# Optimization experiments

Hardware: AMD Instinct MI355X
Metric: run time of the kernel (lower is better)

## Reference

```python
import jax, jax.numpy as jnp
import numpy as np

N_NODES = 50000
N_EDGES = 800000
IN_CH = 128
HID = 64
PROJ = 32


def _gcn_norm(edge_index, n):
    # add self loops, symmetric normalization D^-1/2 (A+I) D^-1/2
    loop = jnp.arange(n, dtype=edge_index.dtype)
    src = jnp.concatenate([edge_index[0], loop])
    dst = jnp.concatenate([edge_index[1], loop])
    deg = jax.ops.segment_sum(jnp.ones_like(dst, jnp.float32), dst, num_segments=n)
    dinv = deg ** -0.5  # deg >= 1 due to self loops
    norm = dinv[src] * dinv[dst]
    return src, dst, norm


def _propagate(h, src, dst, norm, n):
    # gather -> scale -> scatter-add (message passing along A_hat)
    return jax.ops.segment_sum(h[src] * norm[:, None], dst, num_segments=n)


def _ho_gcn_layer(x, src, dst, norm, Ws, b, n):
    # out = sum_{k=1..max_order} (A_hat^k x) W_k + b
    out = jnp.zeros((n, Ws[0].shape[1]), x.dtype)
    h = x
    for W in Ws:
        h = _propagate(h, src, dst, norm, n)
        out = out + h @ W
    return out + b


def setup_inputs() -> dict:
    key = jax.random.key(0)
    ks = jax.random.split(key, 16)

    def w(k, fan_in, fan_out):
        return (jax.random.normal(k, (fan_in, fan_out), jnp.float32) / np.sqrt(fan_in)).astype(jnp.float32)

    x = jax.random.normal(ks[0], (N_NODES, IN_CH), jnp.float32)
    edge_index = jax.random.randint(ks[1], (2, N_EDGES), 0, N_NODES, dtype=jnp.int64)
    return {
        "x": x,
        "edge_index": edge_index,
        # conv1: max_order=2 -> two weights
        "W1_1": w(ks[2], IN_CH, HID), "W1_2": w(ks[3], IN_CH, HID),
        "b1": jnp.zeros((HID,), jnp.float32),
        # conv2
        "W2_1": w(ks[4], HID, HID // 2), "W2_2": w(ks[5], HID, HID // 2),
        "b2": jnp.zeros((HID // 2,), jnp.float32),
        # projection head
        "Wp1": w(ks[6], HID // 2, PROJ), "bp1": jnp.zeros((PROJ,), jnp.float32),
        "Wp2": w(ks[7], PROJ, PROJ), "bp2": jnp.zeros((PROJ,), jnp.float32),
        # coordinate head
        "Wc1": w(ks[8], HID // 2, HID // 4), "bc1": jnp.zeros((HID // 4,), jnp.float32),
        "Wc2": w(ks[9], HID // 4, 2), "bc2": jnp.zeros((2,), jnp.float32),
    }


def reference(x, edge_index, W1_1, W1_2, b1, W2_1, W2_2, b2,
              Wp1, bp1, Wp2, bp2, Wc1, bc1, Wc2, bc2):
    n = x.shape[0]
    src, dst, norm = _gcn_norm(edge_index, n)
    h1 = jax.nn.relu(_ho_gcn_layer(x, src, dst, norm, (W1_1, W1_2), b1, n))
    # dropout is identity in eval/reference mode
    h2 = jax.nn.relu(_ho_gcn_layer(h1, src, dst, norm, (W2_1, W2_2), b2, n))
    z = jax.nn.relu(h2 @ Wp1 + bp1) @ Wp2 + bp2
    coordinates = jax.nn.relu(h2 @ Wc1 + bc1) @ Wc2 + bc2
    return (coordinates, z)
```

## Files before the change

kernel.cpp:

```cpp
#include <hip/hip_runtime.h>

#define NN 50000
#define NE 800000
#define S 4
#define BINW 12500
#define NN4 (NN * S)
#define NBLK2 ((NN4 + 255) / 256)
#define NBG ((NN + 63) / 64)
#define NBH4 ((NE / 4 + 255) / 256)
#define COLCAP (NE + 3 * NN4 + 8)

__global__ __launch_bounds__(256) void zero_cnt_k(int* __restrict__ cnt,
                                                  float* __restrict__ dinv,
                                                  float* __restrict__ y1s,
                                                  float* __restrict__ y2s,
                                                  float* __restrict__ z1s,
                                                  float* __restrict__ z2s) {
    int i = blockIdx.x * blockDim.x + threadIdx.x;
    if (i < NN4) cnt[i] = 0;
    if (blockIdx.x == 0) {
        int t = threadIdx.x;
        if (t < 64) { y1s[t] = 0.f; y2s[t] = 0.f; }
        else if (t < 96) { z1s[t - 64] = 0.f; z2s[t - 64] = 0.f; }
        else if (t == 96) dinv[NN] = 0.f;
    }
}

__global__ __launch_bounds__(256) void hist_k(const int* __restrict__ src,
                                              const int* __restrict__ dst,
                                              int* __restrict__ cnt,
                                              int* __restrict__ rank) {
    int e = (blockIdx.x * 256 + threadIdx.x) * 4;
    if (e >= NE) return;
    int4 s4 = *(const int4*)(src + e);
    int4 d4 = *(const int4*)(dst + e);
    int4 r;
    r.x = atomicAdd(&cnt[d4.x * S + s4.x / BINW], 1);
    r.y = atomicAdd(&cnt[d4.y * S + s4.y / BINW], 1);
    r.z = atomicAdd(&cnt[d4.z * S + s4.z / BINW], 1);
    r.w = atomicAdd(&cnt[d4.w * S + s4.w / BINW], 1);
    *(int4*)(rank + e) = r;
}

__global__ __launch_bounds__(256) void sum_blocks_k(const int* __restrict__ cnt,
                                                    int* __restrict__ bsum,
                                                    float* __restrict__ dinv) {
    __shared__ int s[256];
    int t = threadIdx.x;
    int i = blockIdx.x * 256 + t;
    int v = 0;
    if (i < NN4) {
        int c = cnt[i];
        v = (c + 3) & ~3;
        if ((i & 3) == 0) {
            int deg = c + cnt[i + 1] + cnt[i + 2] + cnt[i + 3];
            dinv[i >> 2] = rsqrtf((float)(deg + 1));
        }
    }
    s[t] = v;
    __syncthreads();
    for (int off = 128; off > 0; off >>= 1) {
        if (t < off) s[t] += s[t + off];
        __syncthreads();
    }
    if (t == 0) bsum[blockIdx.x] = s[0];
}

__global__ __launch_bounds__(256) void scan_final_k(const int* __restrict__ cnt,
                                                    const int* __restrict__ bsum,
                                                    int* __restrict__ rowsS) {
    __shared__ int sOff[256];
    __shared__ int s[256];
    int t = threadIdx.x;
    int accum = 0;
    for (int idx = t; idx < NBLK2; idx += 256)
        if (idx < blockIdx.x) accum += bsum[idx];
    sOff[t] = accum;
    __syncthreads();
    for (int off = 128; off > 0; off >>= 1) {
        if (t < off) sOff[t] += sOff[t + off];
        __syncthreads();
    }
    int boff = sOff[0];

    int i = blockIdx.x * 256 + t;
    int v = (i < NN4) ? ((cnt[i] + 3) & ~3) : 0;
    s[t] = v;
    __syncthreads();
    for (int off = 1; off < 256; off <<= 1) {
        int x = (t >= off) ? s[t - off] : 0;
        __syncthreads();
        s[t] += x;
        __syncthreads();
    }
    if (i < NN4) rowsS[i] = boff + s[t] - v;
    if (blockIdx.x == NBLK2 - 1 && t == 255) rowsS[NN4] = boff + s[t];
}

__global__ __launch_bounds__(256) void gemm1_scatter_k(const float* __restrict__ A,
                                                       const float* __restrict__ WA,
                                                       const float* __restrict__ WB,
                                                       float* __restrict__ outA,
                                                       float* __restrict__ outB,
                                                       const int* __restrict__ src,
                                                       const int* __restrict__ dst,
                                                       const int* __restrict__ rank,
                                                       const int* __restrict__ rowsS,
                                                       const int* __restrict__ cnt,
                                                       int* __restrict__ col) {
    if (blockIdx.x >= NBG) {
        int idx = (blockIdx.x - NBG) * 256 + threadIdx.x;
        int e = idx * 4;
        if (e < NE) {
            int4 s4 = *(const int4*)(src + e);
            int4 d4 = *(const int4*)(dst + e);
            int4 r4 = *(const int4*)(rank + e);
            col[rowsS[d4.x * S + s4.x / BINW] + r4.x] = s4.x;
            col[rowsS[d4.y * S + s4.y / BINW] + r4.y] = s4.y;
            col[rowsS[d4.z * S + s4.z / BINW] + r4.z] = s4.z;
            col[rowsS[d4.w * S + s4.w / BINW] + r4.w] = s4.w;
        }
        if (idx < NN4) {
            int end = rowsS[idx] + cnt[idx];
            int nxt = rowsS[idx + 1];
            for (int i = end; i < nxt; i++) col[i] = NN;
        }
        return;
    }

    __shared__ float As[64 * 36];
    __shared__ float W1s[32 * 68];
    __shared__ float W2s[32 * 68];
    const int t = threadIdx.x;
    const int tj = t & 15;
    const int tn = t >> 4;
    const int n0 = blockIdx.x * 64;
    float acc[4][8] = {};

    for (int kc = 0; kc < 128; kc += 32) {
        if (kc) __syncthreads();
        {
            int idx = t;
#pragma unroll
            for (int r = 0; r < 2; r++, idx += 256) {
                int nl = idx >> 3, q = idx & 7;
                int node = n0 + nl; node = node < NN ? node : NN - 1;
                float4 a = ((const float4*)A)[(size_t)node * 32 + (kc >> 2) + q];
                *(float4*)&As[nl * 36 + q * 4] = a;
            }
        }
        {
            int idx = t;
#pragma unroll
            for (int r = 0; r < 2; r++, idx += 256) {
                int kl = idx >> 4, j4 = idx & 15;
                *(float4*)&W1s[kl * 68 + j4 * 4] = ((const float4*)WA)[(size_t)(kc + kl) * 16 + j4];
                *(float4*)&W2s[kl * 68 + j4 * 4] = ((const float4*)WB)[(size_t)(kc + kl) * 16 + j4];
            }
        }
        __syncthreads();

        const float* ap = &As[tn * 4 * 36];
        const float* w1p = &W1s[tj * 4];
        const float* w2p = &W2s[tj * 4];
#pragma unroll 2
        for (int k4 = 0; k4 < 8; k4++) {
            float4 a0 = *(const float4*)&ap[0 * 36 + k4 * 4];
            float4 a1 = *(const float4*)&ap[1 * 36 + k4 * 4];
            float4 a2 = *(const float4*)&ap[2 * 36 + k4 * 4];
            float4 a3 = *(const float4*)&ap[3 * 36 + k4 * 4];
#pragma unroll
            for (int kk = 0; kk < 4; kk++) {
                float4 w1 = *(const float4*)&w1p[(k4 * 4 + kk) * 68];
                float4 w2 = *(const float4*)&w2p[(k4 * 4 + kk) * 68];
                float av0 = kk == 0 ? a0.x : kk == 1 ? a0.y : kk == 2 ? a0.z : a0.w;
                float av1 = kk == 0 ? a1.x : kk == 1 ? a1.y : kk == 2 ? a1.z : a1.w;
                float av2 = kk == 0 ? a2.x : kk == 1 ? a2.y : kk == 2 ? a2.z : a2.w;
                float av3 = kk == 0 ? a3.x : kk == 1 ? a3.y : kk == 2 ? a3.z : a3.w;
#define FMA8(m, AV)                                                     \
                acc[m][0] += AV * w1.x; acc[m][1] += AV * w1.y;          \
                acc[m][2] += AV * w1.z; acc[m][3] += AV * w1.w;          \
                acc[m][4] += AV * w2.x; acc[m][5] += AV * w2.y;          \
                acc[m][6] += AV * w2.z; acc[m][7] += AV * w2.w;
                FMA8(0, av0)
                FMA8(1, av1)
                FMA8(2, av2)
                FMA8(3, av3)
#undef FMA8
            }
        }
    }

#pragma unroll
    for (int m = 0; m < 4; m++) {
        int node = n0 + tn * 4 + m;
        if (node < NN) {
            *(float4*)&outA[(size_t)node * 64 + tj * 4] =
                make_float4(acc[m][0], acc[m][1], acc[m][2], acc[m][3]);
            *(float4*)&outB[(size_t)node * 64 + tj * 4] =
                make_float4(acc[m][4], acc[m][5], acc[m][6], acc[m][7]);
        }
    }
}

template<int LOG2C4, bool ADDIN>
__global__ __launch_bounds__(256) void prop_k(const float4* __restrict__ h4,
                                              const float4* __restrict__ addin4,
                                              const float* __restrict__ bias,
                                              float4* __restrict__ out4,
                                              const int* __restrict__ rowsS,
                                              const int* __restrict__ col,
                                              const float* __restrict__ dinv) {
    const int C4 = 1 << LOG2C4;
    unsigned tid = blockIdx.x * blockDim.x + threadIdx.x;
    unsigned node = tid >> LOG2C4;
    if (node >= NN) return;
    unsigned lane = tid & (C4 - 1);
    size_t rowoff = ((size_t)node << LOG2C4) + lane;
    float dn = dinv[node];
    float4 hv = h4[rowoff];
    int rs = rowsS[node * S];
    int re = rowsS[node * S + S];
    int4 c = *(const int4*)(col + rs);
    float4 g = make_float4(0.f, 0.f, 0.f, 0.f);
    for (int i = rs; i < re; i += 4) {
        int4 cc = c;
        c = *(const int4*)(col + i + 4);
        float a0 = dinv[cc.x];
        float a1 = dinv[cc.y];
        float a2 = dinv[cc.z];
        float a3 = dinv[cc.w];
        float4 v0 = h4[((size_t)cc.x << LOG2C4) + lane];
        float4 v1 = h4[((size_t)cc.y << LOG2C4) + lane];
        float4 v2 = h4[((size_t)cc.z << LOG2C4) + lane];
        float4 v3 = h4[((size_t)cc.w << LOG2C4) + lane];
        g.x += a0 * v0.x + a1 * v1.x + a2 * v2.x + a3 * v3.x;
        g.y += a0 * v0.y + a1 * v1.y + a2 * v2.y + a3 * v3.y;
        g.z += a0 * v0.z + a1 * v1.z + a2 * v2.z + a3 * v3.z;
        g.w += a0 * v0.w + a1 * v1.w + a2 * v2.w + a3 * v3.w;
    }
    float w0 = dn * dn;
    float4 acc;
    if (ADDIN) {
        float4 a = addin4[rowoff];
        acc.x = a.x + w0 * hv.x + dn * g.x;
        acc.y = a.y + w0 * hv.y + dn * g.y;
        acc.z = a.z + w0 * hv.z + dn * g.z;
        acc.w = a.w + w0 * hv.w + dn * g.w;
    } else {
        float4 b = ((const float4*)bias)[lane];
        acc.x = fmaxf(b.x + w0 * hv.x + dn * g.x, 0.0f);
        acc.y = fmaxf(b.y + w0 * hv.y + dn * g.y, 0.0f);
        acc.z = fmaxf(b.z + w0 * hv.z + dn * g.z, 0.0f);
        acc.w = fmaxf(b.w + w0 * hv.w + dn * g.w, 0.0f);
    }
    out4[rowoff] = acc;
}

template<int K, int JW>
__global__ __launch_bounds__(256) void gemm_k(const float* __restrict__ A,
                                              const float* __restrict__ WA,
                                              const float* __restrict__ WB,
                                              float* __restrict__ outA,
                                              float* __restrict__ outB, int n) {
    __shared__ float As[64 * 68];
    __shared__ float Ws[64 * 68];
    const int t = threadIdx.x;
    const int tj = t & 15;
    const int tn = t >> 4;
    const int n0 = blockIdx.x * 64;
    float acc[4][4] = {};

    for (int kc = 0; kc < K; kc += 64) {
        if (kc) __syncthreads();
        {
            int idx = t;
#pragma unroll
            for (int r = 0; r < 4; r++, idx += 256) {
                int nl = idx >> 4, q = idx & 15;
                int node = n0 + nl; node = node < n ? node : n - 1;
                float4 a = ((const float4*)A)[(size_t)node * (K / 4) + (kc >> 2) + q];
                *(float4*)&As[nl * 68 + q * 4] = a;
            }
        }
        {
            int idx = t;
#pragma unroll
            for (int r = 0; r < 4; r++, idx += 256) {
                int kl = idx >> 4, j4 = idx & 15;
                const float* W = (j4 < 8) ? WA : WB;
                float4 w = ((const float4*)W)[(size_t)(kc + kl) * 8 + (j4 & 7)];
                *(float4*)&Ws[kl * 68 + j4 * 4] = w;
            }
        }
        __syncthreads();

        const float* ap = &As[tn * 4 * 68];
        const float* wp = &Ws[tj * 4];
#pragma unroll 4
        for (int k4 = 0; k4 < 16; k4++) {
            float4 a0 = *(const float4*)&ap[0 * 68 + k4 * 4];
            float4 a1 = *(const float4*)&ap[1 * 68 + k4 * 4];
            float4 a2 = *(const float4*)&ap[2 * 68 + k4 * 4];
            float4 a3 = *(const float4*)&ap[3 * 68 + k4 * 4];
            float4 w0 = *(const float4*)&wp[(k4 * 4 + 0) * 68];
            float4 w1 = *(const float4*)&wp[(k4 * 4 + 1) * 68];
            float4 w2 = *(const float4*)&wp[(k4 * 4 + 2) * 68];
            float4 w3 = *(const float4*)&wp[(k4 * 4 + 3) * 68];
#define FMA_ROW(m, AV)                                                   \
            acc[m][0] += AV.x * w0.x + AV.y * w1.x + AV.z * w2.x + AV.w * w3.x; \
            acc[m][1] += AV.x * w0.y + AV.y * w1.y + AV.z * w2.y + AV.w * w3.y; \
            acc[m][2] += AV.x * w0.z + AV.y * w1.z + AV.z * w2.z + AV.w * w3.z; \
            acc[m][3] += AV.x * w0.w + AV.y * w1.w + AV.z * w2.w + AV.w * w3.w;
            FMA_ROW(0, a0)
            FMA_ROW(1, a1)
            FMA_ROW(2, a2)
            FMA_ROW(3, a3)
#undef FMA_ROW
        }
    }

    float* ob = ((tj >> 3) ? outB : outA) + (tj & 7) * 4;
#pragma unroll
    for (int m = 0; m < 4; m++) {
        int node = n0 + tn * 4 + m;
        if (node < n)
            *(float4*)&ob[(size_t)node * JW] =
                make_float4(acc[m][0], acc[m][1], acc[m][2], acc[m][3]);
    }
}

__global__ __launch_bounds__(256) void heads_k(const float* __restrict__ h2,
                                               const float* __restrict__ Wp1, const float* __restrict__ bp1,
                                               const float* __restrict__ Wp2, const float* __restrict__ bp2,
                                               const float* __restrict__ Wc1, const float* __restrict__ bc1,
                                               const float* __restrict__ Wc2, const float* __restrict__ bc2,
                                               float* __restrict__ coord, float* __restrict__ z, int n) {
    __shared__ float sWp1[32 * 32], sWp2[32 * 32], sWc1[32 * 16], sWc2[32];
    __shared__ float sbp1[32], sbp2[32], sbc1[16], sbc2[2];
    __shared__ float sh[32 * 36], st[32 * 36], stc[32 * 18];
    const int t = threadIdx.x;
    for (int i = t; i < 1024; i += 256) { sWp1[i] = Wp1[i]; sWp2[i] = Wp2[i]; }
    for (int i = t; i < 512; i += 256) sWc1[i] = Wc1[i];
    if (t < 32) { sWc2[t] = Wc2[t]; sbp1[t] = bp1[t]; sbp2[t] = bp2[t]; }
    if (t < 16) sbc1[t] = bc1[t];
    if (t < 2) sbc2[t] = bc2[t];

    const int n0 = blockIdx.x * 32;
    const int nl = t >> 3;
    const int jq = t & 7;
    const int node = n0 + nl;
    {
        float4 v = make_float4(0.f, 0.f, 0.f, 0.f);
        if (node < n) v = *(const float4*)&h2[(size_t)node * 32 + jq * 4];
        *(float4*)&sh[nl * 36 + jq * 4] = v;
    }
    __syncthreads();

    float4 a = *(const float4*)&sbp1[jq * 4];
#pragma unroll
    for (int k = 0; k < 32; k++) {
        float hv = sh[nl * 36 + k];
        float4 w = *(const float4*)&sWp1[k * 32 + jq * 4];
        a.x += hv * w.x; a.y += hv * w.y; a.z += hv * w.z; a.w += hv * w.w;
    }
    a.x = fmaxf(a.x, 0.f); a.y = fmaxf(a.y, 0.f);
    a.z = fmaxf(a.z, 0.f); a.w = fmaxf(a.w, 0.f);
    *(float4*)&st[nl * 36 + jq * 4] = a;

    float2 c = *(const float2*)&sbc1[jq * 2];
#pragma unroll
    for (int k = 0; k < 32; k++) {
        float hv = sh[nl * 36 + k];
        float2 w = *(const float2*)&sWc1[k * 16 + jq * 2];
        c.x += hv * w.x; c.y += hv * w.y;
    }
    c.x = fmaxf(c.x, 0.f); c.y = fmaxf(c.y, 0.f);
    *(float2*)&stc[nl * 18 + jq * 2] = c;
    __syncthreads();

    float4 zz = *(const float4*)&sbp2[jq * 4];
#pragma unroll
    for (int k = 0; k < 32; k++) {
        float tv = st[nl * 36 + k];
        float4 w = *(const float4*)&sWp2[k * 32 + jq * 4];
        zz.x += tv * w.x; zz.y += tv * w.y; zz.z += tv * w.z; zz.w += tv * w.w;
    }
    if (node < n) *(float4*)&z[(size_t)node * 32 + jq * 4] = zz;

    if (jq < 2) {
        float s = sbc2[jq];
#pragma unroll
        for (int k = 0; k < 16; k++) s += stc[nl * 18 + k] * sWc2[k * 2 + jq];
        if (node < n) coord[(size_t)node * 2 + jq] = s;
    }
}

extern "C" void kernel_launch(void* const* d_in, const int* in_sizes, int n_in,
                              void* d_out, int out_size, void* d_ws, size_t ws_size,
                              hipStream_t stream) {
    const float* x    = (const float*)d_in[0];
    const int*   ei   = (const int*)d_in[1];
    const int*   src  = ei;
    const int*   dst  = ei + NE;
    const float* W1_1 = (const float*)d_in[2];
    const float* W1_2 = (const float*)d_in[3];
    const float* b1   = (const float*)d_in[4];
    const float* W2_1 = (const float*)d_in[5];
    const float* W2_2 = (const float*)d_in[6];
    const float* b2   = (const float*)d_in[7];
    const float* Wp1  = (const float*)d_in[8];
    const float* bp1  = (const float*)d_in[9];
    const float* Wp2  = (const float*)d_in[10];
    const float* bp2  = (const float*)d_in[11];
    const float* Wc1  = (const float*)d_in[12];
    const float* bc1  = (const float*)d_in[13];
    const float* Wc2  = (const float*)d_in[14];
    const float* bc2  = (const float*)d_in[15];

    float* ws    = (float*)d_ws;
    float* dinv  = ws;
    int*   cnt   = (int*)(ws + 50004);
    int*   rowsS = cnt + NN4;
    int*   bsum  = rowsS + NN4 + 4;
    int*   rank  = bsum + 1024;
    int*   col   = rank + NE;
    float* bufY  = (float*)(col + COLCAP);
    float* bufZ  = bufY + (size_t)(NN + 1) * 128;

    float* y1 = bufY;
    float* y2 = bufY + (size_t)(NN + 1) * 64;
    float* u  = y1;
    float* h1 = y2;
    float* z1 = bufZ;
    float* z2 = bufZ + (size_t)(NN + 1) * 32;
    float* u2 = z1;
    float* h2 = z2;

    float* coord = (float*)d_out;
    float* z     = (float*)d_out + 2 * NN;

    zero_cnt_k<<<NBLK2, 256, 0, stream>>>(cnt, dinv,
                                          y1 + (size_t)NN * 64, y2 + (size_t)NN * 64,
                                          z1 + (size_t)NN * 32, z2 + (size_t)NN * 32);
    hist_k<<<NBH4, 256, 0, stream>>>(src, dst, cnt, rank);
    sum_blocks_k<<<NBLK2, 256, 0, stream>>>(cnt, bsum, dinv);
    scan_final_k<<<NBLK2, 256, 0, stream>>>(cnt, bsum, rowsS);
    gemm1_scatter_k<<<NBG + NBH4, 256, 0, stream>>>(x, W1_1, W1_2, y1, y2,
                                                    src, dst, rank, rowsS, cnt, col);

    prop_k<4, true><<<(NN * 16 + 255) / 256, 256, 0, stream>>>(
        (const float4*)y2, (const float4*)y1, nullptr, (float4*)u, rowsS, col, dinv);
    prop_k<4, false><<<(NN * 16 + 255) / 256, 256, 0, stream>>>(
        (const float4*)u, nullptr, b1, (float4*)h1, rowsS, col, dinv);
    gemm_k<64, 32><<<(NN + 63) / 64, 256, 0, stream>>>(h1, W2_1, W2_2, z1, z2, NN);
    prop_k<3, true><<<(NN * 8 + 255) / 256, 256, 0, stream>>>(
        (const float4*)z2, (const float4*)z1, nullptr, (float4*)u2, rowsS, col, dinv);
    prop_k<3, false><<<(NN * 8 + 255) / 256, 256, 0, stream>>>(
        (const float4*)u2, nullptr, b2, (float4*)h2, rowsS, col, dinv);
    heads_k<<<(NN + 31) / 32, 256, 0, stream>>>(h2, Wp1, bp1, Wp2, bp2, Wc1, bc1, Wc2, bc2, coord, z, NN);
}
```

Baseline: 285.3 us.

## Pre-scale features by dinv to drop per-edge dinv gathers; fuse last prop into heads

Rows of the propagated features are pre-multiplied by the source-node dinv, either in the GEMM epilogue or in the first propagation's output. This removes the random dinv gather and multiply per edge in every propagation, and the self-loop term folds into the accumulator initialisation. The final propagation is fused into the heads kernel so h2 is never written out and read back. The risks are small floating-point reordering differences and lower parallelism in the fused kernel, since it runs with 32 nodes per block.

```diff
diff --git a/kernel.cpp b/kernel.cpp
--- a/kernel.cpp
+++ b/kernel.cpp
@@ -11,7 +11,6 @@
 #define COLCAP (NE + 3 * NN4 + 8)
 
 __global__ __launch_bounds__(256) void zero_cnt_k(int* __restrict__ cnt,
-                                                  float* __restrict__ dinv,
                                                   float* __restrict__ y1s,
                                                   float* __restrict__ y2s,
                                                   float* __restrict__ z1s,
@@ -22,7 +21,6 @@
         int t = threadIdx.x;
         if (t < 64) { y1s[t] = 0.f; y2s[t] = 0.f; }
         else if (t < 96) { z1s[t - 64] = 0.f; z2s[t - 64] = 0.f; }
-        else if (t == 96) dinv[NN] = 0.f;
     }
 }
 
@@ -107,7 +105,8 @@
                                                        const int* __restrict__ rank,
                                                        const int* __restrict__ rowsS,
                                                        const int* __restrict__ cnt,
-                                                       int* __restrict__ col) {
+                                                       int* __restrict__ col,
+                                                       const float* __restrict__ dinv) {
     if (blockIdx.x >= NBG) {
         int idx = (blockIdx.x - NBG) * 256 + threadIdx.x;
         int e = idx * 4;
@@ -195,10 +194,12 @@
     for (int m = 0; m < 4; m++) {
         int node = n0 + tn * 4 + m;
         if (node < NN) {
+            float dnm = dinv[node];
             *(float4*)&outA[(size_t)node * 64 + tj * 4] =
                 make_float4(acc[m][0], acc[m][1], acc[m][2], acc[m][3]);
             *(float4*)&outB[(size_t)node * 64 + tj * 4] =
-                make_float4(acc[m][4], acc[m][5], acc[m][6], acc[m][7]);
+                make_float4(dnm * acc[m][4], dnm * acc[m][5],
+                            dnm * acc[m][6], dnm * acc[m][7]);
         }
     }
 }
@@ -218,41 +219,35 @@
     unsigned lane = tid & (C4 - 1);
     size_t rowoff = ((size_t)node << LOG2C4) + lane;
     float dn = dinv[node];
-    float4 hv = h4[rowoff];
+    float4 g = h4[rowoff];
     int rs = rowsS[node * S];
     int re = rowsS[node * S + S];
     int4 c = *(const int4*)(col + rs);
-    float4 g = make_float4(0.f, 0.f, 0.f, 0.f);
     for (int i = rs; i < re; i += 4) {
         int4 cc = c;
         c = *(const int4*)(col + i + 4);
-        float a0 = dinv[cc.x];
-        float a1 = dinv[cc.y];
-        float a2 = dinv[cc.z];
-        float a3 = dinv[cc.w];
         float4 v0 = h4[((size_t)cc.x << LOG2C4) + lane];
         float4 v1 = h4[((size_t)cc.y << LOG2C4) + lane];
         float4 v2 = h4[((size_t)cc.z << LOG2C4) + lane];
         float4 v3 = h4[((size_t)cc.w << LOG2C4) + lane];
-        g.x += a0 * v0.x + a1 * v1.x + a2 * v2.x + a3 * v3.x;
-        g.y += a0 * v0.y + a1 * v1.y + a2 * v2.y + a3 * v3.y;
-        g.z += a0 * v0.z + a1 * v1.z + a2 * v2.z + a3 * v3.z;
-        g.w += a0 * v0.w + a1 * v1.w + a2 * v2.w + a3 * v3.w;
-    }
-    float w0 = dn * dn;
+        g.x += v0.x + v1.x + v2.x + v3.x;
+        g.y += v0.y + v1.y + v2.y + v3.y;
+        g.z += v0.z + v1.z + v2.z + v3.z;
+        g.w += v0.w + v1.w + v2.w + v3.w;
+    }
     float4 acc;
     if (ADDIN) {
         float4 a = addin4[rowoff];
-        acc.x = a.x + w0 * hv.x + dn * g.x;
-        acc.y = a.y + w0 * hv.y + dn * g.y;
-        acc.z = a.z + w0 * hv.z + dn * g.z;
-        acc.w = a.w + w0 * hv.w + dn * g.w;
+        acc.x = dn * (a.x + dn * g.x);
+        acc.y = dn * (a.y + dn * g.y);
+        acc.z = dn * (a.z + dn * g.z);
+        acc.w = dn * (a.w + dn * g.w);
     } else {
         float4 b = ((const float4*)bias)[lane];
-        acc.x = fmaxf(b.x + w0 * hv.x + dn * g.x, 0.0f);
-        acc.y = fmaxf(b.y + w0 * hv.y + dn * g.y, 0.0f);
-        acc.z = fmaxf(b.z + w0 * hv.z + dn * g.z, 0.0f);
-        acc.w = fmaxf(b.w + w0 * hv.w + dn * g.w, 0.0f);
+        acc.x = fmaxf(b.x + dn * g.x, 0.0f);
+        acc.y = fmaxf(b.y + dn * g.y, 0.0f);
+        acc.z = fmaxf(b.z + dn * g.z, 0.0f);
+        acc.w = fmaxf(b.w + dn * g.w, 0.0f);
     }
     out4[rowoff] = acc;
 }
@@ -262,7 +257,8 @@
                                               const float* __restrict__ WA,
                                               const float* __restrict__ WB,
                                               float* __restrict__ outA,
-                                              float* __restrict__ outB, int n) {
+                                              float* __restrict__ outB, int n,
+                                              const float* __restrict__ dinv) {
     __shared__ float As[64 * 68];
     __shared__ float Ws[64 * 68];
     const int t = threadIdx.x;
@@ -320,22 +316,30 @@
         }
     }
 
-    float* ob = ((tj >> 3) ? outB : outA) + (tj & 7) * 4;
+    int mat = tj >> 3;
+    float* ob = (mat ? outB : outA) + (tj & 7) * 4;
 #pragma unroll
     for (int m = 0; m < 4; m++) {
         int node = n0 + tn * 4 + m;
-        if (node < n)
+        if (node < n) {
+            float sc = mat ? dinv[node] : 1.0f;
             *(float4*)&ob[(size_t)node * JW] =
-                make_float4(acc[m][0], acc[m][1], acc[m][2], acc[m][3]);
-    }
-}
-
-__global__ __launch_bounds__(256) void heads_k(const float* __restrict__ h2,
-                                               const float* __restrict__ Wp1, const float* __restrict__ bp1,
-                                               const float* __restrict__ Wp2, const float* __restrict__ bp2,
-                                               const float* __restrict__ Wc1, const float* __restrict__ bc1,
-                                               const float* __restrict__ Wc2, const float* __restrict__ bc2,
-                                               float* __restrict__ coord, float* __restrict__ z, int n) {
+                make_float4(sc * acc[m][0], sc * acc[m][1],
+                            sc * acc[m][2], sc * acc[m][3]);
+        }
+    }
+}
+
+__global__ __launch_bounds__(256) void prop_heads_k(const float4* __restrict__ h4,
+                                                    const float* __restrict__ b2,
+                                                    const int* __restrict__ rowsS,
+                                                    const int* __restrict__ col,
+                                                    const float* __restrict__ dinv,
+                                                    const float* __restrict__ Wp1, const float* __restrict__ bp1,
+                                                    const float* __restrict__ Wp2, const float* __restrict__ bp2,
+                                                    const float* __restrict__ Wc1, const float* __restrict__ bc1,
+                                                    const float* __restrict__ Wc2, const float* __restrict__ bc2,
+                                                    float* __restrict__ coord, float* __restrict__ z) {
     __shared__ float sWp1[32 * 32], sWp2[32 * 32], sWc1[32 * 16], sWc2[32];
     __shared__ float sbp1[32], sbp2[32], sbc1[16], sbc2[2];
     __shared__ float sh[32 * 36], st[32 * 36], stc[32 * 18];
@@ -350,11 +354,34 @@
     const int nl = t >> 3;
     const int jq = t & 7;
     const int node = n0 + nl;
-    {
-        float4 v = make_float4(0.f, 0.f, 0.f, 0.f);
-        if (node < n) v = *(const float4*)&h2[(size_t)node * 32 + jq * 4];
-        *(float4*)&sh[nl * 36 + jq * 4] = v;
-    }
+
+    float4 acc = make_float4(0.f, 0.f, 0.f, 0.f);
+    if (node < NN) {
+        size_t rowoff = ((size_t)node << 3) + jq;
+        float dn = dinv[node];
+        float4 g = h4[rowoff];
+        int rs = rowsS[node * S];
+        int re = rowsS[node * S + S];
+        int4 c = *(const int4*)(col + rs);
+        for (int i = rs; i < re; i += 4) {
+            int4 cc = c;
+            c = *(const int4*)(col + i + 4);
+            float4 v0 = h4[((size_t)cc.x << 3) + jq];
+            float4 v1 = h4[((size_t)cc.y << 3) + jq];
+            float4 v2 = h4[((size_t)cc.z << 3) + jq];
+            float4 v3 = h4[((size_t)cc.w << 3) + jq];
+            g.x += v0.x + v1.x + v2.x + v3.x;
+            g.y += v0.y + v1.y + v2.y + v3.y;
+            g.z += v0.z + v1.z + v2.z + v3.z;
+            g.w += v0.w + v1.w + v2.w + v3.w;
+        }
+        float4 b = ((const float4*)b2)[jq];
+        acc.x = fmaxf(b.x + dn * g.x, 0.0f);
+        acc.y = fmaxf(b.y + dn * g.y, 0.0f);
+        acc.z = fmaxf(b.z + dn * g.z, 0.0f);
+        acc.w = fmaxf(b.w + dn * g.w, 0.0f);
+    }
+    *(float4*)&sh[nl * 36 + jq * 4] = acc;
     __syncthreads();
 
     float4 a = *(const float4*)&sbp1[jq * 4];
@@ -368,15 +395,15 @@
     a.z = fmaxf(a.z, 0.f); a.w = fmaxf(a.w, 0.f);
     *(float4*)&st[nl * 36 + jq * 4] = a;
 
-    float2 c = *(const float2*)&sbc1[jq * 2];
+    float2 cc2 = *(const float2*)&sbc1[jq * 2];
 #pragma unroll
     for (int k = 0; k < 32; k++) {
         float hv = sh[nl * 36 + k];
         float2 w = *(const float2*)&sWc1[k * 16 + jq * 2];
-        c.x += hv * w.x; c.y += hv * w.y;
-    }
-    c.x = fmaxf(c.x, 0.f); c.y = fmaxf(c.y, 0.f);
-    *(float2*)&stc[nl * 18 + jq * 2] = c;
+        cc2.x += hv * w.x; cc2.y += hv * w.y;
+    }
+    cc2.x = fmaxf(cc2.x, 0.f); cc2.y = fmaxf(cc2.y, 0.f);
+    *(float2*)&stc[nl * 18 + jq * 2] = cc2;
     __syncthreads();
 
     float4 zz = *(const float4*)&sbp2[jq * 4];
@@ -386,13 +413,13 @@
         float4 w = *(const float4*)&sWp2[k * 32 + jq * 4];
         zz.x += tv * w.x; zz.y += tv * w.y; zz.z += tv * w.z; zz.w += tv * w.w;
     }
-    if (node < n) *(float4*)&z[(size_t)node * 32 + jq * 4] = zz;
+    if (node < NN) *(float4*)&z[(size_t)node * 32 + jq * 4] = zz;
 
     if (jq < 2) {
         float s = sbc2[jq];
 #pragma unroll
         for (int k = 0; k < 16; k++) s += stc[nl * 18 + k] * sWc2[k * 2 + jq];
-        if (node < n) coord[(size_t)node * 2 + jq] = s;
+        if (node < NN) coord[(size_t)node * 2 + jq] = s;
     }
 }
 
@@ -435,28 +462,27 @@
     float* z1 = bufZ;
     float* z2 = bufZ + (size_t)(NN + 1) * 32;
     float* u2 = z1;
-    float* h2 = z2;
 
     float* coord = (float*)d_out;
     float* z     = (float*)d_out + 2 * NN;
 
-    zero_cnt_k<<<NBLK2, 256, 0, stream>>>(cnt, dinv,
+    zero_cnt_k<<<NBLK2, 256, 0, stream>>>(cnt,
                                           y1 + (size_t)NN * 64, y2 + (size_t)NN * 64,
                                           z1 + (size_t)NN * 32, z2 + (size_t)NN * 32);
     hist_k<<<NBH4, 256, 0, stream>>>(src, dst, cnt, rank);
     sum_blocks_k<<<NBLK2, 256, 0, stream>>>(cnt, bsum, dinv);
     scan_final_k<<<NBLK2, 256, 0, stream>>>(cnt, bsum, rowsS);
     gemm1_scatter_k<<<NBG + NBH4, 256, 0, stream>>>(x, W1_1, W1_2, y1, y2,
-                                                    src, dst, rank, rowsS, cnt, col);
+                                                    src, dst, rank, rowsS, cnt, col, dinv);
 
     prop_k<4, true><<<(NN * 16 + 255) / 256, 256, 0, stream>>>(
         (const float4*)y2, (const float4*)y1, nullptr, (float4*)u, rowsS, col, dinv);
     prop_k<4, false><<<(NN * 16 + 255) / 256, 256, 0, stream>>>(
         (const float4*)u, nullptr, b1, (float4*)h1, rowsS, col, dinv);
-    gemm_k<64, 32><<<(NN + 63) / 64, 256, 0, stream>>>(h1, W2_1, W2_2, z1, z2, NN);
+    gemm_k<64, 32><<<(NN + 63) / 64, 256, 0, stream>>>(h1, W2_1, W2_2, z1, z2, NN, dinv);
     prop_k<3, true><<<(NN * 8 + 255) / 256, 256, 0, stream>>>(
         (const float4*)z2, (const float4*)z1, nullptr, (float4*)u2, rowsS, col, dinv);
-    prop_k<3, false><<<(NN * 8 + 255) / 256, 256, 0, stream>>>(
-        (const float4*)u2, nullptr, b2, (float4*)h2, rowsS, col, dinv);
-    heads_k<<<(NN + 31) / 32, 256, 0, stream>>>(h2, Wp1, bp1, Wp2, bp2, Wc1, bc1, Wc2, bc2, coord, z, NN);
-}
+    prop_heads_k<<<(NN + 31) / 32, 256, 0, stream>>>(
+        (const float4*)u2, b2, rowsS, col, dinv,
+        Wp1, bp1, Wp2, bp2, Wc1, bc1, Wc2, bc2, coord, z);
+}
```

Result: faster. 277.7 us (-2.7%).
